# Optimization experiments

Measured on AMD Instinct MI355X. Metric: run time of the kernel, lower is better.

Reference implementation:

```python
import jax, jax.numpy as jnp
import numpy as np

NEG_SLOPE = 0.01  # nn.LeakyReLU default

def leaky_relu(x):
    return jnp.where(x >= 0, x, NEG_SLOPE * x)

def lstm_cell(x, h, c, W_ih, W_hh, b_ih, b_hh):
    # PyTorch LSTMCell: gates ordered i, f, g, o
    gates = x @ W_ih.T + b_ih + h @ W_hh.T + b_hh
    i, f, g, o = jnp.split(gates, 4, axis=-1)
    c_new = jax.nn.sigmoid(f) * c + jax.nn.sigmoid(i) * jnp.tanh(g)
    h_new = jax.nn.sigmoid(o) * jnp.tanh(c_new)
    return h_new, c_new

def setup_inputs() -> dict:
    key = jax.random.key(0)
    B, T, D, H = 2048, 128, 5, 256
    ks = jax.random.split(key, 20)
    s_ih = 1.0 / np.sqrt(H)
    def u(k, shape):
        return jax.random.uniform(k, shape, jnp.float32, -s_ih, s_ih)
    inp = {
        'batch_of_sketches': jax.random.normal(ks[0], (B, T, D), jnp.float32),
        'init_inputs': jax.random.normal(ks[1], (B, D), jnp.float32),
        'W_ih': u(ks[2], (4 * H, D)), 'W_hh': u(ks[3], (4 * H, H)),
        'b_ih': u(ks[4], (4 * H,)), 'b_hh': u(ks[5], (4 * H,)),
        # forward encoder cell
        'W_ih_f': u(ks[6], (4 * H, D)), 'W_hh_f': u(ks[7], (4 * H, H)),
        'b_ih_f': u(ks[8], (4 * H,)), 'b_hh_f': u(ks[9], (4 * H,)),
        # backward encoder cell (dead code in source, kept for fidelity)
        'W_ih_b': u(ks[10], (4 * H, D)), 'W_hh_b': u(ks[11], (4 * H, H)),
        'b_ih_b': u(ks[12], (4 * H,)), 'b_hh_b': u(ks[13], (4 * H,)),
        # linear_encode: 2H -> H ; linear_output: H -> D
        'W_enc': u(ks[14], (H, 2 * H)), 'b_enc': u(ks[15], (H,)),
        'W_out': u(ks[16], (D, H)), 'b_out': u(ks[17], (D,)),
    }
    return inp

def reference(batch_of_sketches, init_inputs,
              W_ih, W_hh, b_ih, b_hh,
              W_ih_f, W_hh_f, b_ih_f, b_hh_f,
              W_ih_b, W_hh_b, b_ih_b, b_hh_b,
              W_enc, b_enc, W_out, b_out):
    B, T, D = batch_of_sketches.shape
    H = W_hh.shape[1]
    dt = batch_of_sketches.dtype

    # ---- encode: forward LSTM over time ----
    def enc_step(carry, x_t):
        h, c = carry
        h, c = lstm_cell(x_t, h, c, W_ih_f, W_hh_f, b_ih_f, b_hh_f)
        return (h, c), None
    xs = jnp.swapaxes(batch_of_sketches, 0, 1)  # [T, B, D]
    (h_f, c_f), _ = jax.lax.scan(enc_step, (jnp.zeros((B, H), dt), jnp.zeros((B, H), dt)), xs)

    # backward loop in source is range(0, cells, -1) -> empty: states stay zero
    h_b = jnp.zeros((B, H), dt)
    c_b = jnp.zeros((B, H), dt)

    h2 = jnp.concatenate([h_f, h_b], axis=1)  # [B, 2H]
    c2 = jnp.concatenate([c_f, c_b], axis=1)
    hidden = leaky_relu(h2 @ W_enc.T + b_enc)
    cell = leaky_relu(c2 @ W_enc.T + b_enc)

    def gen_step(carry, _):
        x, h, c = carry
        h, c = lstm_cell(x, h, c, W_ih, W_hh, b_ih, b_hh)
        out = leaky_relu(h @ W_out.T + b_out)
        return (out, h, c), out
    (_, _, _), outs = jax.lax.scan(gen_step, (init_inputs, hidden, cell), None, length=T)
    return jnp.swapaxes(outs, 0, 1)  # [B, T, D]
```

## Files before the change

### kernel.cpp

```cpp
#include <hip/hip_runtime.h>


typedef __bf16 bf16x8 __attribute__((ext_vector_type(8)));
typedef __bf16 bf16x4 __attribute__((ext_vector_type(4)));
typedef float f32x4 __attribute__((ext_vector_type(4)));
typedef int i32x4 __attribute__((ext_vector_type(4)));

#define MFMA16(A, B, C) __builtin_amdgcn_mfma_f32_16x16x32_bf16((A), (B), (C), 0, 0, 0)

__device__ __forceinline__ float fast_sigmoid(float x) {
  float e = __builtin_amdgcn_exp2f(-1.4426950408889634f * x);
  return __builtin_amdgcn_rcpf(1.0f + e);
}
__device__ __forceinline__ float fast_tanh(float x) {
  float e = __builtin_amdgcn_exp2f(2.8853900817779268f * x);
  return 1.0f - 2.0f * __builtin_amdgcn_rcpf(e + 1.0f);
}
__device__ __forceinline__ float lrelu(float x) { return x >= 0.0f ? x : 0.01f * x; }

__device__ __forceinline__ bf16x8 asbf(i32x4 v) {
  union { i32x4 i; bf16x8 b; } u; u.i = v; return u.b;
}

__global__ void pack_gates_k(const float* __restrict__ Whh, const float* __restrict__ Wih,
                             const float* __restrict__ bih, const float* __restrict__ bhh,
                             __bf16* __restrict__ wpack, __bf16* __restrict__ wih4,
                             __bf16* __restrict__ wihd4, float* __restrict__ bias) {
  int lane = threadIdx.x, blk = blockIdx.x;
  if (blk < 512) {
    int gt = blk >> 3, c = blk & 7;
    int g = gt * 16 + (lane & 15);
    int k0 = c * 32 + (lane >> 4) * 8;
    bf16x8 v;
#pragma unroll
    for (int j = 0; j < 8; ++j) v[j] = (__bf16)Whh[g * 256 + k0 + j];
    *(bf16x8*)(wpack + ((size_t)(gt * 8 + c) * 64 + lane) * 8) = v;
  } else if (blk < 528) {
    int g = (blk - 512) * 64 + lane;
    bf16x4 v;
#pragma unroll
    for (int j = 0; j < 4; ++j) v[j] = (__bf16)Wih[g * 5 + j];
    *(bf16x4*)(wih4 + (size_t)g * 4) = v;
    wihd4[g] = (__bf16)Wih[g * 5 + 4];
  } else {
    int g = (blk - 528) * 64 + lane;
    bias[g] = bih[g] + bhh[g];
  }
}

__global__ void pack_misc_k(const float* __restrict__ Wenc, const float* __restrict__ Wout,
                            __bf16* __restrict__ encpack, __bf16* __restrict__ outd) {
  int lane = threadIdx.x, blk = blockIdx.x;
  if (blk < 128) {
    int T2 = blk >> 3, c = blk & 7;
    int row = T2 * 16 + (lane & 15);
    int k0 = c * 32 + (lane >> 4) * 8;
    bf16x8 v;
#pragma unroll
    for (int j = 0; j < 8; ++j) v[j] = (__bf16)Wenc[row * 512 + k0 + j];
    *(bf16x8*)(encpack + ((size_t)(T2 * 8 + c) * 64 + lane) * 8) = v;
  } else {
    for (int i = lane; i < 1280; i += 64) {
      int row = i >> 8, kk = i & 255;
      outd[row * 256 + (kk ^ (row << 3))] = (__bf16)Wout[row * 256 + kk];
    }
  }
}

#define LOADQ(DST, P, CA, CB)                                                        \
  _Pragma("unroll") for (int q = 0; q < 4; ++q) {                                    \
    const int gtq = q * 16 + ut2 + (P);                                              \
    DST[q] = Ws[(gtq * 8 + (CA)) * 64 + lane];                                       \
    DST[4 + q] = Ws[(gtq * 8 + (CB)) * 64 + lane];                                   \
  }

#define GATEPASS(P, AX, HVP)                                                         \
  {                                                                                  \
    i32x4 s0[8], s1[8];                                                              \
    LOADQ(s0, P, 0, 1);                                                              \
    LOADQ(s1, P, 2, 3);                                                              \
    const int gt0 = 0 * 16 + ut2 + (P), gt1 = 1 * 16 + ut2 + (P);                    \
    const int gt2 = 2 * 16 + ut2 + (P), gt3 = 3 * 16 + ut2 + (P);                    \
    const float bv0 = biass[gt0 * 16 + col], bv1 = biass[gt1 * 16 + col];            \
    const float bv2 = biass[gt2 * 16 + col], bv3 = biass[gt3 * 16 + col];            \
    f32x4 a0 = {bv0, bv0, bv0, bv0}, a1 = {bv1, bv1, bv1, bv1};                      \
    f32x4 a2 = {bv2, bv2, bv2, bv2}, a3 = {bv3, bv3, bv3, bv3};                      \
    {                                                           \
      bf16x8 ac0 = *(const bf16x8*)(hbb + ((col * 512 + 0 * 64 + lgrp * 16) ^ xsw)); \
      a0 = MFMA16(ac0, asbf(s0[0]), a0); a1 = MFMA16(ac0, asbf(s0[1]), a1);          \
      a2 = MFMA16(ac0, asbf(s0[2]), a2); a3 = MFMA16(ac0, asbf(s0[3]), a3);          \
      bf16x8 ac1 = *(const bf16x8*)(hbb + ((col * 512 + 1 * 64 + lgrp * 16) ^ xsw)); \
      a0 = MFMA16(ac1, asbf(s0[4]), a0); a1 = MFMA16(ac1, asbf(s0[5]), a1);          \
      a2 = MFMA16(ac1, asbf(s0[6]), a2); a3 = MFMA16(ac1, asbf(s0[7]), a3);          \
    }                                                                                \
    LOADQ(s0, P, 6, 7);         \
    {                                                           \
      bf16x8 ac2 = *(const bf16x8*)(hbb + ((col * 512 + 2 * 64 + lgrp * 16) ^ xsw)); \
      a0 = MFMA16(ac2, asbf(s1[0]), a0); a1 = MFMA16(ac2, asbf(s1[1]), a1);          \
      a2 = MFMA16(ac2, asbf(s1[2]), a2); a3 = MFMA16(ac2, asbf(s1[3]), a3);          \
      bf16x8 ac3 = *(const bf16x8*)(hbb + ((col * 512 + 3 * 64 + lgrp * 16) ^ xsw)); \
      a0 = MFMA16(ac3, asbf(s1[4]), a0); a1 = MFMA16(ac3, asbf(s1[5]), a1);          \
      a2 = MFMA16(ac3, asbf(s1[6]), a2); a3 = MFMA16(ac3, asbf(s1[7]), a3);          \
    }                                                                                \
    _Pragma("unroll") for (int c2 = 0; c2 < 2; ++c2) {         \
      bf16x8 ac = *(const bf16x8*)(hbb + ((col * 512 + (c2 + 4) * 64 + lgrp * 16) ^ xsw)); \
      a0 = MFMA16(ac, *(const bf16x8*)&wlds[c2][gt0][lane][0], a0);                  \
      a1 = MFMA16(ac, *(const bf16x8*)&wlds[c2][gt1][lane][0], a1);                  \
      a2 = MFMA16(ac, *(const bf16x8*)&wlds[c2][gt2][lane][0], a2);                  \
      a3 = MFMA16(ac, *(const bf16x8*)&wlds[c2][gt3][lane][0], a3);                  \
    }                                                                                \
    {                                                  \
      bf16x8 ac6 = *(const bf16x8*)(hbb + ((col * 512 + 6 * 64 + lgrp * 16) ^ xsw)); \
      a0 = MFMA16(ac6, asbf(s0[0]), a0); a1 = MFMA16(ac6, asbf(s0[1]), a1);          \
      a2 = MFMA16(ac6, asbf(s0[2]), a2); a3 = MFMA16(ac6, asbf(s0[3]), a3);          \
      bf16x8 ac7 = *(const bf16x8*)(hbb + ((col * 512 + 7 * 64 + lgrp * 16) ^ xsw)); \
      a0 = MFMA16(ac7, asbf(s0[4]), a0); a1 = MFMA16(ac7, asbf(s0[5]), a1);          \
      a2 = MFMA16(ac7, asbf(s0[6]), a2); a3 = MFMA16(ac7, asbf(s0[7]), a3);          \
    }                                                                                \
    {                                                              \
      bf16x8 b0f = {}, b1f = {}, b2f = {}, b3f = {};                                 \
      if (lgrp == 0) {                                                               \
        bf16x4 w40 = *(const bf16x4*)&wih4s[gt0 * 16 + col][0];                      \
        bf16x4 w41 = *(const bf16x4*)&wih4s[gt1 * 16 + col][0];                      \
        bf16x4 w42 = *(const bf16x4*)&wih4s[gt2 * 16 + col][0];                      \
        bf16x4 w43 = *(const bf16x4*)&wih4s[gt3 * 16 + col][0];                      \
        b0f[0]=w40[0]; b0f[1]=w40[1]; b0f[2]=w40[2]; b0f[3]=w40[3];                  \
        b1f[0]=w41[0]; b1f[1]=w41[1]; b1f[2]=w41[2]; b1f[3]=w41[3];                  \
        b2f[0]=w42[0]; b2f[1]=w42[1]; b2f[2]=w42[2]; b2f[3]=w42[3];                  \
        b3f[0]=w43[0]; b3f[1]=w43[1]; b3f[2]=w43[2]; b3f[3]=w43[3];                  \
        b0f[4]=wihd4s[gt0 * 16 + col]; b1f[4]=wihd4s[gt1 * 16 + col];                \
        b2f[4]=wihd4s[gt2 * 16 + col]; b3f[4]=wihd4s[gt3 * 16 + col];                \
      }                                                                              \
      a0 = MFMA16(AX, b0f, a0); a1 = MFMA16(AX, b1f, a1);                            \
      a2 = MFMA16(AX, b2f, a2); a3 = MFMA16(AX, b3f, a3);                            \
    }                                                                                \
    _Pragma("unroll") for (int r = 0; r < 4; ++r) {                                  \
      float ig = fast_sigmoid(a0[r]);                                                \
      float fg = fast_sigmoid(a1[r]);                                                \
      float gg = fast_tanh(a2[r]);                                                   \
      float og = fast_sigmoid(a3[r]);                                                \
      float cn = fg * c_reg[P][r] + ig * gg;                                         \
      c_reg[P][r] = cn;                                                              \
      HVP[r] = og * fast_tanh(cn);                                                   \
    }                                                                                \
  }

#define HWRITE2(HV)                                                                    \
  _Pragma("unroll") for (int P = 0; P < 2; ++P)                                        \
  _Pragma("unroll") for (int r = 0; r < 4; ++r) {                                      \
    const int row = lgrp * 4 + r;                                                      \
    const int u = 32 * wv + 16 * P + col;                                              \
    *(__bf16*)(hbb + ((row * 512 + u * 2) ^ ((row & 7) << 4))) = (__bf16)HV[P][r];     \
  }

__global__ __launch_bounds__(512) void rnn_ln(
    const float* __restrict__ sk, const float* __restrict__ initx,
    const i32x4* __restrict__ Wg, const __bf16* __restrict__ Wih4g, const __bf16* __restrict__ Wihd4g,
    const float* __restrict__ Bg,
    const i32x4* __restrict__ Wf, const __bf16* __restrict__ Wih4f, const __bf16* __restrict__ Wihd4f,
    const float* __restrict__ Bf,
    const bf16x8* __restrict__ Epk, const float* __restrict__ benc,
    const __bf16* __restrict__ Od, const float* __restrict__ bout,
    float* __restrict__ out) {
  __shared__ __attribute__((aligned(16))) __bf16 wlds[2][64][64][8];
  __shared__ __attribute__((aligned(16))) __bf16 wih4s[1024][4];
  __shared__ __attribute__((aligned(16))) __bf16 hb[4096];
  __shared__ __attribute__((aligned(16))) float biass[1024];
  __shared__ __attribute__((aligned(16))) __bf16 woutd[5][256];
  __shared__ __attribute__((aligned(16))) __bf16 wihd4s[1024];
  __shared__ __attribute__((aligned(16))) __bf16 xts[8][16][8];

  const int tid = threadIdx.x, lane = tid & 63, wv = tid >> 6;
  const int col = lane & 15, lgrp = lane >> 4;
  const int b0 = blockIdx.x * 16;
  const int ut2 = wv * 2;
  const int xsw = (col & 7) << 4;
  char* hbb = (char*)hb;
  char* wob = (char*)woutd;

  auto stage_wlds = [&](const i32x4* Wpk) {
    for (int i = tid; i < 8192; i += 512) {
      int c2 = i >> 12, gt = (i >> 6) & 63, ln = i & 63;
      *(i32x4*)&wlds[c2][gt][ln][0] = Wpk[(gt * 8 + 4 + c2) * 64 + ln];
    }
  };
  auto stage_small = [&](const __bf16* w4, const __bf16* wd4, const float* Bp) {
    for (int i = tid; i < 1024; i += 512) {
      *(bf16x4*)&wih4s[i][0] = *(const bf16x4*)(w4 + (size_t)i * 4);
      wihd4s[i] = wd4[i];
      biass[i] = Bp[i];
    }
  };

  stage_wlds(Wf);
  stage_small(Wih4f, Wihd4f, Bf);
  for (int i = tid; i < 4096; i += 512) hb[i] = (__bf16)0.0f;
  for (int i = tid; i < 1024; i += 512) (&xts[0][0][0])[i] = (__bf16)0.0f;

  const i32x4* Ws = Wf;

  float c_reg[2][4] = {{0.f, 0.f, 0.f, 0.f}, {0.f, 0.f, 0.f, 0.f}};
  float xc0 = 0.f, xc1 = 0.f, xc2 = 0.f, xc3 = 0.f, xc4 = 0.f;
  if (lgrp == 0) {
    const float* xp = sk + (size_t)(b0 + col) * 128 * 5;
    xc0 = xp[0]; xc1 = xp[1]; xc2 = xp[2]; xc3 = xp[3]; xc4 = xp[4];
  }
  __syncthreads();

#pragma unroll 1
  for (int t = 0; t < 128; ++t) {
    asm volatile("" : "+s"(Ws));
    bf16x8 ax = (bf16x8){};
    if (lgrp == 0) {
      ax[0] = (__bf16)xc0; ax[1] = (__bf16)xc1; ax[2] = (__bf16)xc2;
      ax[3] = (__bf16)xc3; ax[4] = (__bf16)xc4;
    }
    if (t < 127 && lgrp == 0) {
      const float* xp = sk + ((size_t)(b0 + col) * 128 + t + 1) * 5;
      xc0 = xp[0]; xc1 = xp[1]; xc2 = xp[2]; xc3 = xp[3]; xc4 = xp[4];
    }
    float hv[2][4];
    GATEPASS(0, ax, hv[0]);
    GATEPASS(1, ax, hv[1]);
    __syncthreads();
    HWRITE2(hv);
    __syncthreads();
  }

  bf16x8 ah[8];
#pragma unroll
  for (int c = 0; c < 8; ++c)
    ah[c] = *(const bf16x8*)(hbb + ((col * 512 + c * 64 + lgrp * 16) ^ xsw));
  __syncthreads();
#pragma unroll
  for (int P = 0; P < 2; ++P)
#pragma unroll
    for (int r = 0; r < 4; ++r) {
      const int row = lgrp * 4 + r;
      const int u = 32 * wv + 16 * P + col;
      *(__bf16*)(hbb + ((row * 512 + u * 2) ^ ((row & 7) << 4))) = (__bf16)c_reg[P][r];
    }
  __syncthreads();
  bf16x8 acf[8];
#pragma unroll
  for (int c = 0; c < 8; ++c)
    acf[c] = *(const bf16x8*)(hbb + ((col * 512 + c * 64 + lgrp * 16) ^ xsw));
  __syncthreads();

  float hvt[2][4];
#pragma unroll
  for (int p = 0; p < 2; ++p) {
    const int T2 = ut2 + p;
    const float bvh = benc[T2 * 16 + col];
    f32x4 hacc = {bvh, bvh, bvh, bvh};
    f32x4 cacc = {bvh, bvh, bvh, bvh};
#pragma unroll
    for (int c = 0; c < 8; ++c) {
      bf16x8 eb = Epk[(T2 * 8 + c) * 64 + lane];
      hacc = MFMA16(ah[c], eb, hacc);
      cacc = MFMA16(acf[c], eb, cacc);
    }
#pragma unroll
    for (int r = 0; r < 4; ++r) {
      hvt[p][r] = lrelu(hacc[r]);
      c_reg[p][r] = lrelu(cacc[r]);
    }
  }
  HWRITE2(hvt);

  stage_wlds(Wg);
  stage_small(Wih4g, Wihd4g, Bg);
  for (int i = tid; i < 1280; i += 512) (&woutd[0][0])[i] = Od[i];
  Ws = Wg;

  const float bo = (col < 5) ? bout[col] : 0.0f;
  bf16x8 ax = (bf16x8){};
  if (lgrp == 0) {
    const float* xp = initx + (size_t)(b0 + col) * 5;
    ax[0] = (__bf16)xp[0]; ax[1] = (__bf16)xp[1]; ax[2] = (__bf16)xp[2];
    ax[3] = (__bf16)xp[3]; ax[4] = (__bf16)xp[4];
  }
  __syncthreads();

  const int orow = (col < 5) ? col : 0;
#pragma unroll 1
  for (int j = 0; j < 128; ++j) {
    asm volatile("" : "+s"(Ws));
    float hv[2][4];
    GATEPASS(0, ax, hv[0]);
    GATEPASS(1, ax, hv[1]);
    __syncthreads();
    HWRITE2(hv);
    __syncthreads();
    f32x4 oacc = {bo, bo, bo, bo};
#pragma unroll
    for (int c = 0; c < 8; ++c) {
      bf16x8 ac = *(const bf16x8*)(hbb + ((col * 512 + c * 64 + lgrp * 16) ^ xsw));
      bf16x8 wb = *(const bf16x8*)(wob + (orow * 512 + ((c * 64 + lgrp * 16) ^ (orow << 4))));
      oacc = MFMA16(ac, wb, oacc);
    }
    if (col < 5) {
#pragma unroll
      for (int r = 0; r < 4; ++r) {
        float v = lrelu(oacc[r]);
        if (wv == 0) out[((size_t)(b0 + lgrp * 4 + r) * 128 + j) * 5 + col] = v;
        xts[wv][lgrp * 4 + r][col] = (__bf16)v;
      }
    }
    ax = (bf16x8){};
    if (lgrp == 0) ax = *(const bf16x8*)&xts[wv][col][0];
  }
}

extern "C" void kernel_launch(void* const* d_in, const int* in_sizes, int n_in,
                              void* d_out, int out_size, void* d_ws, size_t ws_size,
                              hipStream_t stream) {
  const float* sk = (const float*)d_in[0];
  const float* initx = (const float*)d_in[1];
  const float* W_ih = (const float*)d_in[2];
  const float* W_hh = (const float*)d_in[3];
  const float* b_ih = (const float*)d_in[4];
  const float* b_hh = (const float*)d_in[5];
  const float* W_ih_f = (const float*)d_in[6];
  const float* W_hh_f = (const float*)d_in[7];
  const float* b_ih_f = (const float*)d_in[8];
  const float* b_hh_f = (const float*)d_in[9];
  const float* W_enc = (const float*)d_in[14];
  const float* b_enc = (const float*)d_in[15];
  const float* W_out = (const float*)d_in[16];
  const float* b_out = (const float*)d_in[17];

  char* ws = (char*)d_ws;
  __bf16* Wg = (__bf16*)(ws + 0);
  __bf16* Wf = (__bf16*)(ws + 524288);
  __bf16* Wih4g = (__bf16*)(ws + 1048576);
  __bf16* Wihd4g = (__bf16*)(ws + 1056768);
  __bf16* Wih4f = (__bf16*)(ws + 1058816);
  __bf16* Wihd4f = (__bf16*)(ws + 1067008);
  float* Bg = (float*)(ws + 1069056);
  float* Bf = (float*)(ws + 1073152);
  __bf16* Epk = (__bf16*)(ws + 1077248);
  __bf16* Od = (__bf16*)(ws + 1208320);

  pack_gates_k<<<544, 64, 0, stream>>>(W_hh, W_ih, b_ih, b_hh, Wg, Wih4g, Wihd4g, Bg);
  pack_gates_k<<<544, 64, 0, stream>>>(W_hh_f, W_ih_f, b_ih_f, b_hh_f, Wf, Wih4f, Wihd4f, Bf);
  pack_misc_k<<<129, 64, 0, stream>>>(W_enc, W_out, Epk, Od);

  rnn_ln<<<128, 512, 0, stream>>>(
      sk, initx,
      (const i32x4*)Wg, Wih4g, Wihd4g, Bg,
      (const i32x4*)Wf, Wih4f, Wihd4f, Bf,
      (const bf16x8*)Epk, b_enc,
      Od, b_out,
      (float*)d_out);
}
```

Measured before the change: 1.131 ms.

## Split gate work across 16 waves per block instead of 8

Doubles the block to 1024 threads so each wave computes one 16-unit hidden tile instead of two, halving per-wave MFMA and weight-load work per timestep in both the encoder and generator loops. This aims to shorten the serial per-step critical path of the recurrent loop by exposing more wave-level parallelism. In exchange, each step's barriers must now synchronise 16 waves, the per-wave register budget is tighter under the larger launch bound, and more waves contend for LDS and L2 weight bandwidth.

```diff
diff --git a/kernel.cpp b/kernel.cpp
--- a/kernel.cpp
+++ b/kernel.cpp
@@ -67,20 +67,20 @@
   }
 }
 
-#define LOADQ(DST, P, CA, CB)                                                        \
+#define LOADQ(DST, CA, CB)                                                           \
   _Pragma("unroll") for (int q = 0; q < 4; ++q) {                                    \
-    const int gtq = q * 16 + ut2 + (P);                                              \
+    const int gtq = q * 16 + wv;                                                     \
     DST[q] = Ws[(gtq * 8 + (CA)) * 64 + lane];                                       \
     DST[4 + q] = Ws[(gtq * 8 + (CB)) * 64 + lane];                                   \
   }
 
-#define GATEPASS(P, AX, HVP)                                                         \
+#define GATEPASS(AX, HV)                                                             \
   {                                                                                  \
     i32x4 s0[8], s1[8];                                                              \
-    LOADQ(s0, P, 0, 1);                                                              \
-    LOADQ(s1, P, 2, 3);                                                              \
-    const int gt0 = 0 * 16 + ut2 + (P), gt1 = 1 * 16 + ut2 + (P);                    \
-    const int gt2 = 2 * 16 + ut2 + (P), gt3 = 3 * 16 + ut2 + (P);                    \
+    LOADQ(s0, 0, 1);                                                                 \
+    LOADQ(s1, 2, 3);                                                                 \
+    const int gt0 = 0 * 16 + wv, gt1 = 1 * 16 + wv;                                  \
+    const int gt2 = 2 * 16 + wv, gt3 = 3 * 16 + wv;                                  \
     const float bv0 = biass[gt0 * 16 + col], bv1 = biass[gt1 * 16 + col];            \
     const float bv2 = biass[gt2 * 16 + col], bv3 = biass[gt3 * 16 + col];            \
     f32x4 a0 = {bv0, bv0, bv0, bv0}, a1 = {bv1, bv1, bv1, bv1};                      \
@@ -93,7 +93,7 @@
       a0 = MFMA16(ac1, asbf(s0[4]), a0); a1 = MFMA16(ac1, asbf(s0[5]), a1);          \
       a2 = MFMA16(ac1, asbf(s0[6]), a2); a3 = MFMA16(ac1, asbf(s0[7]), a3);          \
     }                                                                                \
-    LOADQ(s0, P, 6, 7);         \
+    LOADQ(s0, 6, 7);                                    \
     {                                                           \
       bf16x8 ac2 = *(const bf16x8*)(hbb + ((col * 512 + 2 * 64 + lgrp * 16) ^ xsw)); \
       a0 = MFMA16(ac2, asbf(s1[0]), a0); a1 = MFMA16(ac2, asbf(s1[1]), a1);          \
@@ -139,21 +139,20 @@
       float fg = fast_sigmoid(a1[r]);                                                \
       float gg = fast_tanh(a2[r]);                                                   \
       float og = fast_sigmoid(a3[r]);                                                \
-      float cn = fg * c_reg[P][r] + ig * gg;                                         \
-      c_reg[P][r] = cn;                                                              \
-      HVP[r] = og * fast_tanh(cn);                                                   \
-    }                                                                                \
-  }
-
-#define HWRITE2(HV)                                                                    \
-  _Pragma("unroll") for (int P = 0; P < 2; ++P)                                        \
+      float cn = fg * c_reg[r] + ig * gg;                                            \
+      c_reg[r] = cn;                                                                 \
+      HV[r] = og * fast_tanh(cn);                                                    \
+    }                                                                                \
+  }
+
+#define HWRITE(HV)                                                                     \
   _Pragma("unroll") for (int r = 0; r < 4; ++r) {                                      \
     const int row = lgrp * 4 + r;                                                      \
-    const int u = 32 * wv + 16 * P + col;                                              \
-    *(__bf16*)(hbb + ((row * 512 + u * 2) ^ ((row & 7) << 4))) = (__bf16)HV[P][r];     \
-  }
-
-__global__ __launch_bounds__(512) void rnn_ln(
+    const int u = wv * 16 + col;                                                       \
+    *(__bf16*)(hbb + ((row * 512 + u * 2) ^ ((row & 7) << 4))) = (__bf16)(HV[r]);      \
+  }
+
+__global__ __launch_bounds__(1024) void rnn_w16(
     const float* __restrict__ sk, const float* __restrict__ initx,
     const i32x4* __restrict__ Wg, const __bf16* __restrict__ Wih4g, const __bf16* __restrict__ Wihd4g,
     const float* __restrict__ Bg,
@@ -168,24 +167,23 @@
   __shared__ __attribute__((aligned(16))) float biass[1024];
   __shared__ __attribute__((aligned(16))) __bf16 woutd[5][256];
   __shared__ __attribute__((aligned(16))) __bf16 wihd4s[1024];
-  __shared__ __attribute__((aligned(16))) __bf16 xts[8][16][8];
+  __shared__ __attribute__((aligned(16))) __bf16 xts[16][16][8];
 
   const int tid = threadIdx.x, lane = tid & 63, wv = tid >> 6;
   const int col = lane & 15, lgrp = lane >> 4;
   const int b0 = blockIdx.x * 16;
-  const int ut2 = wv * 2;
   const int xsw = (col & 7) << 4;
   char* hbb = (char*)hb;
   char* wob = (char*)woutd;
 
   auto stage_wlds = [&](const i32x4* Wpk) {
-    for (int i = tid; i < 8192; i += 512) {
+    for (int i = tid; i < 8192; i += 1024) {
       int c2 = i >> 12, gt = (i >> 6) & 63, ln = i & 63;
       *(i32x4*)&wlds[c2][gt][ln][0] = Wpk[(gt * 8 + 4 + c2) * 64 + ln];
     }
   };
   auto stage_small = [&](const __bf16* w4, const __bf16* wd4, const float* Bp) {
-    for (int i = tid; i < 1024; i += 512) {
+    for (int i = tid; i < 1024; i += 1024) {
       *(bf16x4*)&wih4s[i][0] = *(const bf16x4*)(w4 + (size_t)i * 4);
       wihd4s[i] = wd4[i];
       biass[i] = Bp[i];
@@ -194,12 +192,12 @@
 
   stage_wlds(Wf);
   stage_small(Wih4f, Wihd4f, Bf);
-  for (int i = tid; i < 4096; i += 512) hb[i] = (__bf16)0.0f;
-  for (int i = tid; i < 1024; i += 512) (&xts[0][0][0])[i] = (__bf16)0.0f;
+  for (int i = tid; i < 4096; i += 1024) hb[i] = (__bf16)0.0f;
+  for (int i = tid; i < 2048; i += 1024) (&xts[0][0][0])[i] = (__bf16)0.0f;
 
   const i32x4* Ws = Wf;
 
-  float c_reg[2][4] = {{0.f, 0.f, 0.f, 0.f}, {0.f, 0.f, 0.f, 0.f}};
+  float c_reg[4] = {0.f, 0.f, 0.f, 0.f};
   float xc0 = 0.f, xc1 = 0.f, xc2 = 0.f, xc3 = 0.f, xc4 = 0.f;
   if (lgrp == 0) {
     const float* xp = sk + (size_t)(b0 + col) * 128 * 5;
@@ -219,11 +217,10 @@
       const float* xp = sk + ((size_t)(b0 + col) * 128 + t + 1) * 5;
       xc0 = xp[0]; xc1 = xp[1]; xc2 = xp[2]; xc3 = xp[3]; xc4 = xp[4];
     }
-    float hv[2][4];
-    GATEPASS(0, ax, hv[0]);
-    GATEPASS(1, ax, hv[1]);
+    float hv[4];
+    GATEPASS(ax, hv);
     __syncthreads();
-    HWRITE2(hv);
+    HWRITE(hv);
     __syncthreads();
   }
 
@@ -232,14 +229,7 @@
   for (int c = 0; c < 8; ++c)
     ah[c] = *(const bf16x8*)(hbb + ((col * 512 + c * 64 + lgrp * 16) ^ xsw));
   __syncthreads();
-#pragma unroll
-  for (int P = 0; P < 2; ++P)
-#pragma unroll
-    for (int r = 0; r < 4; ++r) {
-      const int row = lgrp * 4 + r;
-      const int u = 32 * wv + 16 * P + col;
-      *(__bf16*)(hbb + ((row * 512 + u * 2) ^ ((row & 7) << 4))) = (__bf16)c_reg[P][r];
-    }
+  HWRITE(c_reg);
   __syncthreads();
   bf16x8 acf[8];
 #pragma unroll
@@ -247,10 +237,8 @@
     acf[c] = *(const bf16x8*)(hbb + ((col * 512 + c * 64 + lgrp * 16) ^ xsw));
   __syncthreads();
 
-  float hvt[2][4];
-#pragma unroll
-  for (int p = 0; p < 2; ++p) {
-    const int T2 = ut2 + p;
+  {
+    const int T2 = wv;
     const float bvh = benc[T2 * 16 + col];
     f32x4 hacc = {bvh, bvh, bvh, bvh};
     f32x4 cacc = {bvh, bvh, bvh, bvh};
@@ -260,17 +248,18 @@
       hacc = MFMA16(ah[c], eb, hacc);
       cacc = MFMA16(acf[c], eb, cacc);
     }
+    float hvt[4];
 #pragma unroll
     for (int r = 0; r < 4; ++r) {
-      hvt[p][r] = lrelu(hacc[r]);
-      c_reg[p][r] = lrelu(cacc[r]);
-    }
-  }
-  HWRITE2(hvt);
+      hvt[r] = lrelu(hacc[r]);
+      c_reg[r] = lrelu(cacc[r]);
+    }
+    HWRITE(hvt);
+  }
 
   stage_wlds(Wg);
   stage_small(Wih4g, Wihd4g, Bg);
-  for (int i = tid; i < 1280; i += 512) (&woutd[0][0])[i] = Od[i];
+  for (int i = tid; i < 1280; i += 1024) (&woutd[0][0])[i] = Od[i];
   Ws = Wg;
 
   const float bo = (col < 5) ? bout[col] : 0.0f;
@@ -286,11 +275,10 @@
 #pragma unroll 1
   for (int j = 0; j < 128; ++j) {
     asm volatile("" : "+s"(Ws));
-    float hv[2][4];
-    GATEPASS(0, ax, hv[0]);
-    GATEPASS(1, ax, hv[1]);
+    float hv[4];
+    GATEPASS(ax, hv);
     __syncthreads();
-    HWRITE2(hv);
+    HWRITE(hv);
     __syncthreads();
     f32x4 oacc = {bo, bo, bo, bo};
 #pragma unroll
@@ -346,7 +334,7 @@
   pack_gates_k<<<544, 64, 0, stream>>>(W_hh_f, W_ih_f, b_ih_f, b_hh_f, Wf, Wih4f, Wihd4f, Bf);
   pack_misc_k<<<129, 64, 0, stream>>>(W_enc, W_out, Epk, Od);
 
-  rnn_ln<<<128, 512, 0, stream>>>(
+  rnn_w16<<<128, 1024, 0, stream>>>(
       sk, initx,
       (const i32x4*)Wg, Wih4g, Wihd4g, Bg,
       (const i32x4*)Wf, Wih4f, Wihd4f, Bf,
```

Measured after the change: 1.228 ms. 8.5% more time.
